# Kernel optimization log

Hardware: AMD Instinct MI355X
Metric: run time of the kernel (lower is better)

## Reference

```python
import jax, jax.numpy as jnp
import numpy as np


def setup_inputs() -> dict:
    key = jax.random.key(0)
    k1, k2 = jax.random.split(key)
    completed = jax.random.normal(k1, (8, 8192, 3), dtype=jnp.float32)
    partial = jax.random.normal(k2, (8, 4096, 3), dtype=jnp.float32)
    return {"completed": completed, "partial": partial}


def reference(completed, partial) -> jnp.ndarray:
    # torch.cdist(partial, completed): (B, M, N) pairwise Euclidean distances
    # d^2 = ||p||^2 + ||c||^2 - 2 p.c  (computed via GEMM, matching cdist math)
    p_sq = jnp.sum(partial * partial, axis=-1, keepdims=True)          # (B, M, 1)
    c_sq = jnp.sum(completed * completed, axis=-1, keepdims=True)       # (B, N, 1)
    cross = jnp.einsum("bmd,bnd->bmn", partial, completed)             # (B, M, N)
    d2 = p_sq + jnp.swapaxes(c_sq, 1, 2) - 2.0 * cross                  # (B, M, N)
    dist = jnp.sqrt(jnp.maximum(d2, 0.0))
    min_dist = jnp.min(dist, axis=2)                                    # (B, M)
    return jnp.mean(min_dist)
```

## Files before the change

### kernel.cpp

```cpp
#include <hip/hip_runtime.h>


constexpr int B  = 8;
constexpr int N  = 8192;
constexpr int M  = 4096;
constexpr int NT = 256;
constexpr int TP = 8;
constexpr int MBLK = NT * TP;
constexpr int MC   = M / MBLK;
constexpr int NBLK = 256;
constexpr int NC   = N / NBLK;
constexpr int ROWS = B * M;
constexpr float FMAX = 3.402823466e38f;

__global__ __launch_bounds__(NT, 4) void pml_main(const float* __restrict__ completed,
                                                  const float* __restrict__ partial,
                                                  float* __restrict__ ws,
                                                  float* __restrict__ out) {
    __shared__ float4 cs[NBLK];
    const int t     = threadIdx.x;
    const int b     = blockIdx.z;
    const int mBase = blockIdx.y * MBLK;
    const int nBase = blockIdx.x * NBLK;

    if (blockIdx.x == 0 && blockIdx.y == 0 && b == 0 && t == 0)
        out[0] = 0.0f;

    {
        const float* cp = completed + (size_t)(b * N + nBase + t) * 3;
        float x = cp[0], y = cp[1], z = cp[2];
        cs[t] = make_float4(x, y, z, 0.5f * (x * x + y * y + z * z));
    }
    __syncthreads();

    const int m0 = mBase + t * TP;
    const float4* pv = (const float4*)(partial + (size_t)(b * M + m0) * 3);
    float4 v0 = pv[0], v1 = pv[1], v2 = pv[2], v3 = pv[3], v4 = pv[4], v5 = pv[5];

    float nx[TP], ny[TP], nz[TP], fm[TP];
    nx[0] = -v0.x; ny[0] = -v0.y; nz[0] = -v0.z;
    nx[1] = -v0.w; ny[1] = -v1.x; nz[1] = -v1.y;
    nx[2] = -v1.z; ny[2] = -v1.w; nz[2] = -v2.x;
    nx[3] = -v2.y; ny[3] = -v2.z; nz[3] = -v2.w;
    nx[4] = -v3.x; ny[4] = -v3.y; nz[4] = -v3.z;
    nx[5] = -v3.w; ny[5] = -v4.x; nz[5] = -v4.y;
    nx[6] = -v4.z; ny[6] = -v4.w; nz[6] = -v5.x;
    nx[7] = -v5.y; ny[7] = -v5.z; nz[7] = -v5.w;
#pragma unroll
    for (int p = 0; p < TP; ++p) fm[p] = FMAX;

#pragma unroll 4
    for (int j = 0; j < NBLK; j += 2) {
        float4 c0 = cs[j];
        float4 c1 = cs[j + 1];
#pragma unroll
        for (int p = 0; p < TP; ++p) {
            float f0 = fmaf(nx[p], c0.x, fmaf(ny[p], c0.y, fmaf(nz[p], c0.z, c0.w)));
            float f1 = fmaf(nx[p], c1.x, fmaf(ny[p], c1.y, fmaf(nz[p], c1.z, c1.w)));
            fm[p] = fminf(fm[p], fminf(f0, f1));
        }
    }

    float4* wsv = (float4*)(ws + (size_t)blockIdx.x * ROWS + b * M + m0);
    wsv[0] = make_float4(fm[0], fm[1], fm[2], fm[3]);
    wsv[1] = make_float4(fm[4], fm[5], fm[6], fm[7]);
}

constexpr int RT = 256;
constexpr int RBLOCKS = ROWS / RT;

__global__ __launch_bounds__(RT) void pml_reduce(const float* __restrict__ ws,
                                                 const float* __restrict__ partial,
                                                 float* __restrict__ out) {
    const int row = blockIdx.x * RT + threadIdx.x;
    float m0 = FMAX, m1 = FMAX;
#pragma unroll
    for (int c = 0; c < NC; c += 2) {
        float f0 = ws[(size_t)c * ROWS + row];
        float f1 = ws[(size_t)(c + 1) * ROWS + row];
        m0 = fminf(m0, fminf(f0, f1));
    }
    float m = fminf(m0, m1);

    const float* pp = partial + (size_t)row * 3;
    float x = pp[0], y = pp[1], z = pp[2];
    float psq = x * x + y * y + z * z;
    float d2  = fmaxf(fmaf(2.0f, m, psq), 0.0f);
    float s   = sqrtf(d2);

#pragma unroll
    for (int off = 32; off > 0; off >>= 1) s += __shfl_down(s, off);

    __shared__ float red[RT / 64];
    const int lane = threadIdx.x & 63;
    const int wid  = threadIdx.x >> 6;
    if (lane == 0) red[wid] = s;
    __syncthreads();
    if (threadIdx.x == 0) {
        float tot = red[0] + red[1] + red[2] + red[3];
        atomicAdd(out, tot * (1.0f / (float)ROWS));
    }
}

extern "C" void kernel_launch(void* const* d_in, const int* in_sizes, int n_in,
                              void* d_out, int out_size, void* d_ws, size_t ws_size,
                              hipStream_t stream) {
    const float* completed = (const float*)d_in[0];
    const float* partial   = (const float*)d_in[1];
    float* out = (float*)d_out;
    float* ws  = (float*)d_ws;

    dim3 grid(NC, MC, B);
    pml_main<<<grid, NT, 0, stream>>>(completed, partial, ws, out);
    pml_reduce<<<RBLOCKS, RT, 0, stream>>>(ws, partial, out);
}
```

Baseline: 80.04 us.

## Halve column tile per block and vectorize reduce kernel with float4 rows

```diff
diff --git a/kernel.cpp b/kernel.cpp
--- a/kernel.cpp
+++ b/kernel.cpp
@@ -8,7 +8,7 @@
 constexpr int TP = 8;
 constexpr int MBLK = NT * TP;
 constexpr int MC   = M / MBLK;
-constexpr int NBLK = 256;
+constexpr int NBLK = 128;
 constexpr int NC   = N / NBLK;
 constexpr int ROWS = B * M;
 constexpr float FMAX = 3.402823466e38f;
@@ -26,7 +26,7 @@
     if (blockIdx.x == 0 && blockIdx.y == 0 && b == 0 && t == 0)
         out[0] = 0.0f;
 
-    {
+    if (t < NBLK) {
         const float* cp = completed + (size_t)(b * N + nBase + t) * 3;
         float x = cp[0], y = cp[1], z = cp[2];
         cs[t] = make_float4(x, y, z, 0.5f * (x * x + y * y + z * z));
@@ -66,40 +66,44 @@
     wsv[1] = make_float4(fm[4], fm[5], fm[6], fm[7]);
 }
 
-constexpr int RT = 256;
-constexpr int RBLOCKS = ROWS / RT;
+constexpr int RT      = 64;
+constexpr int RQUADS  = ROWS / 4;
+constexpr int RBLOCKS = RQUADS / RT;
 
 __global__ __launch_bounds__(RT) void pml_reduce(const float* __restrict__ ws,
                                                  const float* __restrict__ partial,
                                                  float* __restrict__ out) {
-    const int row = blockIdx.x * RT + threadIdx.x;
-    float m0 = FMAX, m1 = FMAX;
-#pragma unroll
-    for (int c = 0; c < NC; c += 2) {
-        float f0 = ws[(size_t)c * ROWS + row];
-        float f1 = ws[(size_t)(c + 1) * ROWS + row];
-        m0 = fminf(m0, fminf(f0, f1));
+    const int q = blockIdx.x * RT + threadIdx.x;
+    const float4* wsv = (const float4*)ws;
+
+    float4 m = make_float4(FMAX, FMAX, FMAX, FMAX);
+#pragma unroll 16
+    for (int c = 0; c < NC; ++c) {
+        float4 v = wsv[(size_t)c * RQUADS + q];
+        m.x = fminf(m.x, v.x);
+        m.y = fminf(m.y, v.y);
+        m.z = fminf(m.z, v.z);
+        m.w = fminf(m.w, v.w);
     }
-    float m = fminf(m0, m1);
 
-    const float* pp = partial + (size_t)row * 3;
-    float x = pp[0], y = pp[1], z = pp[2];
-    float psq = x * x + y * y + z * z;
-    float d2  = fmaxf(fmaf(2.0f, m, psq), 0.0f);
-    float s   = sqrtf(d2);
+    const float4* pp = (const float4*)partial + (size_t)q * 3;
+    float4 a = pp[0], bb = pp[1], cc = pp[2];
+
+    float psq0 = a.x * a.x + a.y * a.y + a.z * a.z;
+    float psq1 = a.w * a.w + bb.x * bb.x + bb.y * bb.y;
+    float psq2 = bb.z * bb.z + bb.w * bb.w + cc.x * cc.x;
+    float psq3 = cc.y * cc.y + cc.z * cc.z + cc.w * cc.w;
+
+    float s = sqrtf(fmaxf(fmaf(2.0f, m.x, psq0), 0.0f))
+            + sqrtf(fmaxf(fmaf(2.0f, m.y, psq1), 0.0f))
+            + sqrtf(fmaxf(fmaf(2.0f, m.z, psq2), 0.0f))
+            + sqrtf(fmaxf(fmaf(2.0f, m.w, psq3), 0.0f));
 
 #pragma unroll
     for (int off = 32; off > 0; off >>= 1) s += __shfl_down(s, off);
 
-    __shared__ float red[RT / 64];
-    const int lane = threadIdx.x & 63;
-    const int wid  = threadIdx.x >> 6;
-    if (lane == 0) red[wid] = s;
-    __syncthreads();
-    if (threadIdx.x == 0) {
-        float tot = red[0] + red[1] + red[2] + red[3];
-        atomicAdd(out, tot * (1.0f / (float)ROWS));
-    }
+    if (threadIdx.x == 0)
+        atomicAdd(out, s * (1.0f / (float)ROWS));
 }
 
 extern "C" void kernel_launch(void* const* d_in, const int* in_sizes, int n_in,
```

After: 82.71 us. 3.3% more time.

## Replace brute-force distance search with x-binned nearest-neighbour search and pruning

Applied to the files above, without the earlier changes.

```diff
diff --git a/kernel.cpp b/kernel.cpp
--- a/kernel.cpp
+++ b/kernel.cpp
@@ -4,102 +4,136 @@
 constexpr int B  = 8;
 constexpr int N  = 8192;
 constexpr int M  = 4096;
-constexpr int NT = 256;
-constexpr int TP = 8;
-constexpr int MBLK = NT * TP;
-constexpr int MC   = M / MBLK;
-constexpr int NBLK = 256;
-constexpr int NC   = N / NBLK;
+constexpr int NB = 256;
+constexpr float XLO = -6.0f, XHI = 6.0f;
+constexpr float BINW = (XHI - XLO) / NB;
+constexpr float BINV = (float)NB / (XHI - XLO);
 constexpr int ROWS = B * M;
 constexpr float FMAX = 3.402823466e38f;
 
-__global__ __launch_bounds__(NT, 4) void pml_main(const float* __restrict__ completed,
-                                                  const float* __restrict__ partial,
-                                                  float* __restrict__ ws,
-                                                  float* __restrict__ out) {
-    __shared__ float4 cs[NBLK];
-    const int t     = threadIdx.x;
-    const int b     = blockIdx.z;
-    const int mBase = blockIdx.y * MBLK;
-    const int nBase = blockIdx.x * NBLK;
+constexpr size_t OFF_CPK = 16 * 1024;
+constexpr size_t OFF_QPK = OFF_CPK + (size_t)B * N * 16;
 
-    if (blockIdx.x == 0 && blockIdx.y == 0 && b == 0 && t == 0)
-        out[0] = 0.0f;
+__device__ __forceinline__ int binOf(float x) {
+    int k = (int)floorf((x - XLO) * BINV);
+    return k < 0 ? 0 : (k > NB - 1 ? NB - 1 : k);
+}
 
-    {
-        const float* cp = completed + (size_t)(b * N + nBase + t) * 3;
-        float x = cp[0], y = cp[1], z = cp[2];
-        cs[t] = make_float4(x, y, z, 0.5f * (x * x + y * y + z * z));
+__global__ __launch_bounds__(256) void pml_prep(const float* __restrict__ completed,
+                                                const float* __restrict__ partial,
+                                                int* __restrict__ cStart,
+                                                float4* __restrict__ cPk,
+                                                float4* __restrict__ qPk,
+                                                float* __restrict__ out) {
+    __shared__ int cnt[NB];
+    __shared__ int st[NB + 1];
+    const int t    = threadIdx.x;
+    const int role = blockIdx.x;
+    const int b    = role >> 1;
+    const bool isQ = role & 1;
+    const int n    = isQ ? M : N;
+    const float* src = isQ ? partial + (size_t)b * M * 3
+                           : completed + (size_t)b * N * 3;
+
+    for (int k = t; k < NB; k += 256) cnt[k] = 0;
+    __syncthreads();
+    for (int i = t; i < n; i += 256)
+        atomicAdd(&cnt[binOf(src[3 * i])], 1);
+    __syncthreads();
+    if (t == 0) {
+        int acc = 0;
+        for (int k = 0; k < NB; ++k) { st[k] = acc; acc += cnt[k]; }
+        st[NB] = acc;
     }
     __syncthreads();
+    if (!isQ)
+        for (int k = t; k <= NB; k += 256) cStart[b * (NB + 1) + k] = st[k];
+    for (int k = t; k < NB; k += 256) cnt[k] = 0;
+    __syncthreads();
+    for (int i = t; i < n; i += 256) {
+        float x = src[3 * i], y = src[3 * i + 1], z = src[3 * i + 2];
+        int k = binOf(x);
+        int pos = st[k] + atomicAdd(&cnt[k], 1);
+        if (isQ) qPk[(size_t)b * M + pos] = make_float4(x, y, z, x * x + y * y + z * z);
+        else     cPk[(size_t)b * N + pos] = make_float4(x, y, z, 0.5f * (x * x + y * y + z * z));
+    }
+    if (role == 0 && t == 0) out[0] = 0.0f;
+}
 
-    const int m0 = mBase + t * TP;
-    const float4* pv = (const float4*)(partial + (size_t)(b * M + m0) * 3);
-    float4 v0 = pv[0], v1 = pv[1], v2 = pv[2], v3 = pv[3], v4 = pv[4], v5 = pv[5];
+constexpr int SPLIT = 4;
+constexpr int MT = 256;
+constexpr int MAIN_BLOCKS = ROWS * SPLIT / MT;
 
-    float nx[TP], ny[TP], nz[TP], fm[TP];
-    nx[0] = -v0.x; ny[0] = -v0.y; nz[0] = -v0.z;
-    nx[1] = -v0.w; ny[1] = -v1.x; nz[1] = -v1.y;
-    nx[2] = -v1.z; ny[2] = -v1.w; nz[2] = -v2.x;
-    nx[3] = -v2.y; ny[3] = -v2.z; nz[3] = -v2.w;
-    nx[4] = -v3.x; ny[4] = -v3.y; nz[4] = -v3.z;
-    nx[5] = -v3.w; ny[5] = -v4.x; nz[5] = -v4.y;
-    nx[6] = -v4.z; ny[6] = -v4.w; nz[6] = -v5.x;
-    nx[7] = -v5.y; ny[7] = -v5.z; nz[7] = -v5.w;
-#pragma unroll
-    for (int p = 0; p < TP; ++p) fm[p] = FMAX;
+__global__ __launch_bounds__(MT) void pml_main(const int* __restrict__ cStart,
+                                               const float4* __restrict__ cPk,
+                                               const float4* __restrict__ qPk,
+                                               float* __restrict__ out) {
+    const int g   = blockIdx.x * MT + threadIdx.x;
+    const int sub = g & (SPLIT - 1);
+    const int q   = g >> 2;
+    const int b   = q >> 12;
+    const int qi  = q & (M - 1);
 
-#pragma unroll 4
-    for (int j = 0; j < NBLK; j += 2) {
-        float4 c0 = cs[j];
-        float4 c1 = cs[j + 1];
-#pragma unroll
-        for (int p = 0; p < TP; ++p) {
-            float f0 = fmaf(nx[p], c0.x, fmaf(ny[p], c0.y, fmaf(nz[p], c0.z, c0.w)));
-            float f1 = fmaf(nx[p], c1.x, fmaf(ny[p], c1.y, fmaf(nz[p], c1.z, c1.w)));
-            fm[p] = fminf(fm[p], fminf(f0, f1));
+    const float4 Q = qPk[(size_t)b * M + qi];
+    const float px = -Q.x, py = -Q.y, pz = -Q.z, psq = Q.w;
+    const int ib = binOf(Q.x);
+    const int* bs = cStart + b * (NB + 1);
+    const float4* cb = cPk + (size_t)b * N;
+
+    float best = FMAX;
+    {
+        const int e = bs[ib + 1];
+        for (int i = bs[ib] + sub; i < e; i += SPLIT) {
+            float4 c = cb[i];
+            float f = fmaf(px, c.x, fmaf(py, c.y, fmaf(pz, c.z, c.w)));
+            best = fminf(best, f);
         }
     }
-
-    float4* wsv = (float4*)(ws + (size_t)blockIdx.x * ROWS + b * M + m0);
-    wsv[0] = make_float4(fm[0], fm[1], fm[2], fm[3]);
-    wsv[1] = make_float4(fm[4], fm[5], fm[6], fm[7]);
-}
-
-constexpr int RT = 256;
-constexpr int RBLOCKS = ROWS / RT;
-
-__global__ __launch_bounds__(RT) void pml_reduce(const float* __restrict__ ws,
-                                                 const float* __restrict__ partial,
-                                                 float* __restrict__ out) {
-    const int row = blockIdx.x * RT + threadIdx.x;
-    float m0 = FMAX, m1 = FMAX;
-#pragma unroll
-    for (int c = 0; c < NC; c += 2) {
-        float f0 = ws[(size_t)c * ROWS + row];
-        float f1 = ws[(size_t)(c + 1) * ROWS + row];
-        m0 = fminf(m0, fminf(f0, f1));
+    int l = ib - 1, r = ib + 1;
+    bool dL = (l < 0), dR = (r >= NB);
+    while (!(dL && dR)) {
+        float bs4 = fminf(best, __shfl_xor(best, 1));
+        bs4 = fminf(bs4, __shfl_xor(bs4, 2));
+        const float d2 = fmaxf(fmaf(2.0f, bs4, psq), 0.0f);
+        if (!dR) {
+            float gap = fmaf((float)r, BINW, XLO) - Q.x;
+            if (gap * gap >= d2) dR = true;
+            else {
+                const int e = bs[r + 1];
+                for (int i = bs[r] + sub; i < e; i += SPLIT) {
+                    float4 c = cb[i];
+                    float f = fmaf(px, c.x, fmaf(py, c.y, fmaf(pz, c.z, c.w)));
+                    best = fminf(best, f);
+                }
+                if (++r >= NB) dR = true;
+            }
+        }
+        if (!dL) {
+            float gap = Q.x - fmaf((float)(l + 1), BINW, XLO);
+            if (gap * gap >= d2) dL = true;
+            else {
+                const int e = bs[l + 1];
+                for (int i = bs[l] + sub; i < e; i += SPLIT) {
+                    float4 c = cb[i];
+                    float f = fmaf(px, c.x, fmaf(py, c.y, fmaf(pz, c.z, c.w)));
+                    best = fminf(best, f);
+                }
+                if (--l < 0) dL = true;
+            }
+        }
     }
-    float m = fminf(m0, m1);
-
-    const float* pp = partial + (size_t)row * 3;
-    float x = pp[0], y = pp[1], z = pp[2];
-    float psq = x * x + y * y + z * z;
-    float d2  = fmaxf(fmaf(2.0f, m, psq), 0.0f);
-    float s   = sqrtf(d2);
+    best = fminf(best, __shfl_xor(best, 1));
+    best = fminf(best, __shfl_xor(best, 2));
+    float s = (sub == 0) ? sqrtf(fmaxf(fmaf(2.0f, best, psq), 0.0f)) : 0.0f;
 
 #pragma unroll
     for (int off = 32; off > 0; off >>= 1) s += __shfl_down(s, off);
-
-    __shared__ float red[RT / 64];
-    const int lane = threadIdx.x & 63;
-    const int wid  = threadIdx.x >> 6;
+    __shared__ float red[MT / 64];
+    const int lane = threadIdx.x & 63, wid = threadIdx.x >> 6;
     if (lane == 0) red[wid] = s;
     __syncthreads();
-    if (threadIdx.x == 0) {
-        float tot = red[0] + red[1] + red[2] + red[3];
-        atomicAdd(out, tot * (1.0f / (float)ROWS));
-    }
+    if (threadIdx.x == 0)
+        atomicAdd(out, (red[0] + red[1] + red[2] + red[3]) * (1.0f / (float)ROWS));
 }
 
 extern "C" void kernel_launch(void* const* d_in, const int* in_sizes, int n_in,
@@ -108,9 +142,12 @@
     const float* completed = (const float*)d_in[0];
     const float* partial   = (const float*)d_in[1];
     float* out = (float*)d_out;
-    float* ws  = (float*)d_ws;
+    char*  ws  = (char*)d_ws;
 
-    dim3 grid(NC, MC, B);
-    pml_main<<<grid, NT, 0, stream>>>(completed, partial, ws, out);
-    pml_reduce<<<RBLOCKS, RT, 0, stream>>>(ws, partial, out);
+    int*    cStart = (int*)ws;
+    float4* cPk    = (float4*)(ws + OFF_CPK);
+    float4* qPk    = (float4*)(ws + OFF_QPK);
+
+    pml_prep<<<2 * B, 256, 0, stream>>>(completed, partial, cStart, cPk, qPk, out);
+    pml_main<<<MAIN_BLOCKS, MT, 0, stream>>>(cStart, cPk, qPk, out);
 }
```

Result: slower. 291.9 us (+264.7%).
